# Kernel optimization log

Measured on AMD Instinct MI355X. Metric: run time of the kernel, lower is better.

The kernel has to match this reference:

```python
import jax, jax.numpy as jnp
import numpy as np

G, N_PER, D, H, L, IN_DIM = 128, 256, 256, 8, 3, 128
DH = D // H
EPS = 1e-5


def _ln(x, g, b):
    mu = jnp.mean(x, axis=-1, keepdims=True)
    var = jnp.mean(jnp.square(x - mu), axis=-1, keepdims=True)
    return (x - mu) * jax.lax.rsqrt(var + EPS) * g + b


def setup_inputs() -> dict:
    key = jax.random.key(0)
    ks = jax.random.split(key, 16)
    N = G * N_PER
    s = 0.02
    inp = {
        "x": jax.random.normal(ks[0], (N, IN_DIM), dtype=jnp.float32),
        "edge_index": jax.random.randint(ks[1], (2, 16 * N), 0, N, dtype=jnp.int32),
        "batch": (jnp.arange(N, dtype=jnp.int32) // N_PER),
        # input projection
        "Wp": jax.random.normal(ks[2], (D, IN_DIM), dtype=jnp.float32) * s,
        "bp": jnp.zeros((D,), jnp.float32),
        # per-layer stacked params (leading dim L)
        "in_w": jax.random.normal(ks[3], (L, 3 * D, D), dtype=jnp.float32) * s,
        "in_b": jnp.zeros((L, 3 * D), jnp.float32),
        "out_w": jax.random.normal(ks[4], (L, D, D), dtype=jnp.float32) * s,
        "out_b": jnp.zeros((L, D), jnp.float32),
        "n1_g": jnp.ones((L, D), jnp.float32),
        "n1_b": jnp.zeros((L, D), jnp.float32),
        "W1": jax.random.normal(ks[5], (L, 2 * D, D), dtype=jnp.float32) * s,
        "b1": jnp.zeros((L, 2 * D), jnp.float32),
        "W2": jax.random.normal(ks[6], (L, D, 2 * D), dtype=jnp.float32) * s,
        "b2": jnp.zeros((L, D), jnp.float32),
        "n2_g": jnp.ones((L, D), jnp.float32),
        "n2_b": jnp.zeros((L, D), jnp.float32),
        # final LayerNorm
        "ln_g": jnp.ones((D,), jnp.float32),
        "ln_b": jnp.zeros((D,), jnp.float32),
    }
    return inp


def _forward(x, Wp, bp, in_w, in_b, out_w, out_b, n1_g, n1_b, W1, b1, W2, b2, n2_g, n2_b, ln_g, ln_b):
    h = x @ Wp.T + bp                       # [N, D]
    h = h.reshape(G, N_PER, D)              # graphs are contiguous, equal size
    scale = 1.0 / np.sqrt(DH)
    for l in range(L):
        qkv = h @ in_w[l].T + in_b[l]       # [G, n, 3D]
        q, k, v = jnp.split(qkv, 3, axis=-1)
        q = q.reshape(G, N_PER, H, DH)
        k = k.reshape(G, N_PER, H, DH)
        v = v.reshape(G, N_PER, H, DH)
        scores = jnp.einsum('gqhd,gkhd->ghqk', q, k) * scale  # block-diag per graph
        attn = jax.nn.softmax(scores, axis=-1)
        o = jnp.einsum('ghqk,gkhd->gqhd', attn, v).reshape(G, N_PER, D)
        o = o @ out_w[l].T + out_b[l]
        h = _ln(h + o, n1_g[l], n1_b[l])
        f = jax.nn.relu(h @ W1[l].T + b1[l]) @ W2[l].T + b2[l]
        h = _ln(h + f, n2_g[l], n2_b[l])
    h = h.reshape(G * N_PER, D)
    return _ln(h, ln_g, ln_b)


def reference(x, edge_index, batch, Wp, bp, in_w, in_b, out_w, out_b, n1_g, n1_b, W1, b1, W2, b2, n2_g, n2_b, ln_g, ln_b):
    # edge_index and batch structure are honored: graphs are contiguous runs of
    # N_PER nodes, so the per-graph attention loop becomes batched block-diagonal attention.
    del edge_index, batch
    return _forward(x, Wp, bp, in_w, in_b, out_w, out_b, n1_g, n1_b, W1, b1, W2, b2, n2_g, n2_b, ln_g, ln_b)
```

## Files before the change

kernel.cpp:

```cpp
#include <hip/hip_runtime.h>

typedef unsigned short u16;
typedef unsigned long long u64;
typedef short bf16x8 __attribute__((ext_vector_type(8)));
typedef float f32x4 __attribute__((ext_vector_type(4)));

__device__ __forceinline__ u16 f2bf(float f) {
  union { float f; unsigned u; } v; v.f = f;
  unsigned r = v.u + 0x7fffu + ((v.u >> 16) & 1u);
  return (u16)(r >> 16);
}

__device__ __forceinline__ float bf2f(u16 b) {
  union { unsigned u; float f; } v; v.u = ((unsigned)b) << 16;
  return v.f;
}

__device__ __forceinline__ u64 pack4(float x, float y, float z, float w) {
  return (u64)f2bf(x) | ((u64)f2bf(y) << 16) |
         ((u64)f2bf(z) << 32) | ((u64)f2bf(w) << 48);
}

__device__ __forceinline__ float fexp2(float x) {
  float r; asm("v_exp_f32 %0, %1" : "=v"(r) : "v"(x)); return r;
}
__device__ __forceinline__ float frcp(float x) {
  float r; asm("v_rcp_f32 %0, %1" : "=v"(r) : "v"(x)); return r;
}

__device__ __forceinline__ void gld_lds16(const u16* g, u16* l) {
  __builtin_amdgcn_global_load_lds(
      (const __attribute__((address_space(1))) void*)g,
      (__attribute__((address_space(3))) void*)l, 16, 0, 0);
}

#define QSCALE (0.17677669529663687f * 1.44269504088896340f)

template<int MODE>
__global__ __launch_bounds__(256) void gemm_bt(
    const u16* __restrict__ A, const u16* __restrict__ B,
    const float* __restrict__ bias,
    u16* __restrict__ outb,
    int N, int K)
{
  __shared__ u16 As[128 * 64];
  __shared__ u16 Bs[128 * 64];
  const int tid = threadIdx.x;
  const int wave = tid >> 6, lane = tid & 63;
  const int quad = lane >> 4, l16 = lane & 15;

  const int nwg = gridDim.x * gridDim.y;
  int bid = blockIdx.y * gridDim.x + blockIdx.x;
  bid = (bid & 7) * (nwg >> 3) + (bid >> 3);
  const int by = bid / gridDim.x;
  const int bx = bid - by * gridDim.x;
  const int m0 = by * 128, n0 = bx * 128;

  const int wm = (wave >> 1) * 64, wn = (wave & 1) * 64;

  const int r0 = tid >> 3, ch0 = tid & 7;
  const int sc = ((ch0 ^ (r0 & 7)) * 8);

  const f32x4 zero = {0.f, 0.f, 0.f, 0.f};
  f32x4 acc[4][4];
#pragma unroll
  for (int i = 0; i < 4; i++)
#pragma unroll
    for (int j = 0; j < 4; j++) acc[i][j] = zero;

  const u16* Ap = A + (size_t)(m0 + r0) * K + sc;
  const u16* Bp = B + (size_t)(n0 + r0) * K + sc;
  u16* Asd = &As[tid * 8];
  u16* Bsd = &Bs[tid * 8];

  const int swz = (l16 & 7);

  for (int kt = 0; kt < K; kt += 64) {
#pragma unroll
    for (int p = 0; p < 4; p++) {
      gld_lds16(Ap + (size_t)(p * 32) * K + kt, Asd + p * 2048);
      gld_lds16(Bp + (size_t)(p * 32) * K + kt, Bsd + p * 2048);
    }
    __syncthreads();
#pragma unroll
    for (int kk = 0; kk < 2; kk++) {
      const int co = ((kk * 4 + quad) ^ swz) * 8;
      bf16x8 a[4], b[4];
#pragma unroll
      for (int i = 0; i < 4; i++)
        a[i] = *(const bf16x8*)&As[(wm + i * 16 + l16) * 64 + co];
#pragma unroll
      for (int j = 0; j < 4; j++)
        b[j] = *(const bf16x8*)&Bs[(wn + j * 16 + l16) * 64 + co];
#pragma unroll
      for (int i = 0; i < 4; i++)
#pragma unroll
        for (int j = 0; j < 4; j++)
          acc[i][j] = __builtin_amdgcn_mfma_f32_16x16x32_bf16(a[i], b[j], acc[i][j], 0, 0, 0);
    }
    __syncthreads();
  }

  float bj[4];
#pragma unroll
  for (int j = 0; j < 4; j++) bj[j] = bias[n0 + wn + j * 16 + l16];

#pragma unroll
  for (int i = 0; i < 4; i++) {
    const int Rb = m0 + wm + i * 16 + quad * 4;
#pragma unroll
    for (int r = 0; r < 4; r++) {
      const size_t ro = (size_t)(Rb + r) * N;
#pragma unroll
      for (int j = 0; j < 4; j++) {
        const int C = n0 + wn + j * 16 + l16;
        float v = acc[i][j][r] + bj[j];
        if (MODE == 1) {
          if (n0 + wn + j * 16 < 256) v *= QSCALE;
          outb[ro + C] = f2bf(v);
        } else if (MODE == 0) {
          outb[ro + C] = f2bf(v);
        } else {
          outb[ro + C] = f2bf(v > 0.f ? v : 0.f);
        }
      }
    }
  }
}

template<int FINAL>
__global__ __launch_bounds__(256) void gemm_ln(
    const u16* __restrict__ A, const u16* __restrict__ B,
    const float* __restrict__ bias, const u16* __restrict__ resb,
    const float* __restrict__ g1, const float* __restrict__ b1,
    const float* __restrict__ g2, const float* __restrict__ b2,
    float* __restrict__ outf, u16* __restrict__ outb,
    int K)
{
  __shared__ u16 As[64 * 64];
  __shared__ u16 Bs[256 * 64];
  __shared__ float Pp[FINAL ? 5 * 256 : 3 * 256];

  const int tid = threadIdx.x;
  const int wave = tid >> 6, lane = tid & 63;
  const int quad = lane >> 4, l16 = lane & 15;
  const int m0 = blockIdx.x * 64;

  if (tid < 256) {
    Pp[tid] = bias[tid];
    Pp[256 + tid] = g1[tid];
    Pp[512 + tid] = b1[tid];
    if (FINAL) {
      Pp[768 + tid] = g2[tid];
      Pp[1024 + tid] = b2[tid];
    }
  }

  const f32x4 zero = {0.f, 0.f, 0.f, 0.f};
  f32x4 acc[16];
#pragma unroll
  for (int j = 0; j < 16; j++) acc[j] = zero;

  const int r0 = tid >> 3, ch0 = tid & 7;
  const int sc = ((ch0 ^ (r0 & 7)) * 8);
  const u16* Ap = A + (size_t)(m0 + r0) * K + sc;
  const u16* Bp = B + (size_t)r0 * K + sc;
  u16* Asd = &As[tid * 8];
  u16* Bsd = &Bs[tid * 8];
  const int swz = (l16 & 7);

  for (int kt = 0; kt < K; kt += 64) {
#pragma unroll
    for (int p = 0; p < 2; p++)
      gld_lds16(Ap + (size_t)(p * 32) * K + kt, Asd + p * 2048);
#pragma unroll
    for (int p = 0; p < 8; p++)
      gld_lds16(Bp + (size_t)(p * 32) * K + kt, Bsd + p * 2048);
    __syncthreads();
#pragma unroll
    for (int kk = 0; kk < 2; kk++) {
      const int co = ((kk * 4 + quad) ^ swz) * 8;
      bf16x8 af = *(const bf16x8*)&As[(wave * 16 + l16) * 64 + co];
#pragma unroll
      for (int j = 0; j < 16; j++) {
        bf16x8 wf = *(const bf16x8*)&Bs[(j * 16 + l16) * 64 + co];
        acc[j] = __builtin_amdgcn_mfma_f32_16x16x32_bf16(wf, af, acc[j], 0, 0, 0);
      }
    }
    __syncthreads();
  }

  const int row = m0 + wave * 16 + l16;
  const int c4 = quad * 4;
  float s = 0.f, q = 0.f;
#pragma unroll
  for (int j = 0; j < 16; j++) {
    ushort4 rv = *(const ushort4*)(resb + (size_t)row * 256 + j * 16 + c4);
    float4 bv = *(const float4*)(Pp + j * 16 + c4);
    acc[j][0] += bv.x + bf2f(rv.x);
    acc[j][1] += bv.y + bf2f(rv.y);
    acc[j][2] += bv.z + bf2f(rv.z);
    acc[j][3] += bv.w + bf2f(rv.w);
    s += (acc[j][0] + acc[j][1]) + (acc[j][2] + acc[j][3]);
    q += (acc[j][0] * acc[j][0] + acc[j][1] * acc[j][1]) +
         (acc[j][2] * acc[j][2] + acc[j][3] * acc[j][3]);
  }
  s += __shfl_xor(s, 16, 64); s += __shfl_xor(s, 32, 64);
  q += __shfl_xor(q, 16, 64); q += __shfl_xor(q, 32, 64);
  float mu = s * 0.00390625f;
  float rs = rsqrtf(q * 0.00390625f - mu * mu + 1e-5f);

  if (FINAL == 0) {
#pragma unroll
    for (int j = 0; j < 16; j++) {
      float4 gv = *(const float4*)(Pp + 256 + j * 16 + c4);
      float4 bv = *(const float4*)(Pp + 512 + j * 16 + c4);
      float4 y;
      y.x = (acc[j][0] - mu) * rs * gv.x + bv.x;
      y.y = (acc[j][1] - mu) * rs * gv.y + bv.y;
      y.z = (acc[j][2] - mu) * rs * gv.z + bv.z;
      y.w = (acc[j][3] - mu) * rs * gv.w + bv.w;
      const size_t off = (size_t)row * 256 + j * 16 + c4;
      *(u64*)(outb + off) = pack4(y.x, y.y, y.z, y.w);
    }
  } else {
    float s2 = 0.f, q2 = 0.f;
#pragma unroll
    for (int j = 0; j < 16; j++) {
      float4 gv = *(const float4*)(Pp + 256 + j * 16 + c4);
      float4 bv = *(const float4*)(Pp + 512 + j * 16 + c4);
      acc[j][0] = (acc[j][0] - mu) * rs * gv.x + bv.x;
      acc[j][1] = (acc[j][1] - mu) * rs * gv.y + bv.y;
      acc[j][2] = (acc[j][2] - mu) * rs * gv.z + bv.z;
      acc[j][3] = (acc[j][3] - mu) * rs * gv.w + bv.w;
      s2 += (acc[j][0] + acc[j][1]) + (acc[j][2] + acc[j][3]);
      q2 += (acc[j][0] * acc[j][0] + acc[j][1] * acc[j][1]) +
            (acc[j][2] * acc[j][2] + acc[j][3] * acc[j][3]);
    }
    s2 += __shfl_xor(s2, 16, 64); s2 += __shfl_xor(s2, 32, 64);
    q2 += __shfl_xor(q2, 16, 64); q2 += __shfl_xor(q2, 32, 64);
    float mu2 = s2 * 0.00390625f;
    float rs2 = rsqrtf(q2 * 0.00390625f - mu2 * mu2 + 1e-5f);
#pragma unroll
    for (int j = 0; j < 16; j++) {
      float4 gv = *(const float4*)(Pp + 768 + j * 16 + c4);
      float4 bv = *(const float4*)(Pp + 1024 + j * 16 + c4);
      float4 z;
      z.x = (acc[j][0] - mu2) * rs2 * gv.x + bv.x;
      z.y = (acc[j][1] - mu2) * rs2 * gv.y + bv.y;
      z.z = (acc[j][2] - mu2) * rs2 * gv.z + bv.z;
      z.w = (acc[j][3] - mu2) * rs2 * gv.w + bv.w;
      *(float4*)(outf + (size_t)row * 256 + j * 16 + c4) = z;
    }
  }
}

__global__ __launch_bounds__(256) void attn_k(
    const u16* __restrict__ qkv, u16* __restrict__ ob)
{
  __shared__ u16 Ks[256 * 32];
  __shared__ u16 Vt[32 * 256];
  __shared__ u16 Pw[4][16 * 64];

  const int tid = threadIdx.x;
  const int wave = tid >> 6, lane = tid & 63;
  const int quad = lane >> 4, l16 = lane & 15;
  const int g = blockIdx.x >> 3, h = blockIdx.x & 7;
  const int node0 = g << 8;
  const int qoff = h * 32, koff = 256 + h * 32, voff = 512 + h * 32;

  {
    const int kr = tid >> 2, kc = (tid & 3) * 8;
    const u16* Kp = qkv + (size_t)(node0 + kr) * 768 + koff + kc;
    u16* Kd = &Ks[tid * 8];
#pragma unroll
    for (int pass = 0; pass < 4; pass++)
      gld_lds16(Kp + (size_t)pass * 64 * 768, Kd + pass * 2048);
  }

  {
    const int d = lane & 31;
    const int kb2 = lane >> 5;
#pragma unroll
    for (int t = 0; t < 4; t++) {
      const int kbg = wave * 8 + t * 2 + kb2;
      u16 vals[8];
#pragma unroll
      for (int i = 0; i < 8; i++)
        vals[i] = qkv[(size_t)(node0 + kbg * 8 + i) * 768 + voff + d];
      *(bf16x8*)&Vt[d * 256 + ((kbg ^ (d & 7)) << 3)] = *(bf16x8*)vals;
    }
  }

  __syncthreads();

  const f32x4 zero = {0.f, 0.f, 0.f, 0.f};
  bf16x8 ones;
#pragma unroll
  for (int i = 0; i < 8; i++) ones[i] = (short)0x3F80;
  u16* pw = Pw[wave];

  for (int qc = 0; qc < 4; qc++) {
    const int q0 = qc * 64 + wave * 16;

    bf16x8 qf = *(const bf16x8*)&qkv[(size_t)(node0 + q0 + l16) * 768 + qoff + quad * 8];

    f32x4 o[2] = {zero, zero};
    f32x4 ls = zero;

#pragma unroll
    for (int half = 0; half < 2; half++) {
      f32x4 s[8];
      __builtin_amdgcn_s_setprio(1);
#pragma unroll
      for (int ib = 0; ib < 8; ib++) {
        bf16x8 kf = *(const bf16x8*)&Ks[(half * 128 + ib * 16 + l16) * 32 + quad * 8];
        s[ib] = __builtin_amdgcn_mfma_f32_16x16x32_bf16(kf, qf, zero, 0, 0, 0);
      }
      __builtin_amdgcn_s_setprio(0);

#pragma unroll
      for (int Q = 0; Q < 2; Q++) {
#pragma unroll
        for (int ib = 0; ib < 4; ib++) {
          f32x4 p;
#pragma unroll
          for (int r = 0; r < 4; r++) p[r] = fexp2(s[Q * 4 + ib][r]);
          union { float f; unsigned u; } u0, u1, u2, u3;
          u0.f = p[0]; u1.f = p[1]; u2.f = p[2]; u3.f = p[3];
          uint2 pk;
          pk.x = __builtin_amdgcn_perm(u1.u, u0.u, 0x07060302u);
          pk.y = __builtin_amdgcn_perm(u3.u, u2.u, 0x07060302u);
          const int c = 2 * ib + (quad >> 1);
          *(uint2*)&pw[l16 * 64 + ((c ^ (l16 & 7)) << 3) + (quad & 1) * 4] = pk;
        }
#pragma unroll
        for (int ks = 0; ks < 2; ks++) {
          bf16x8 pf = *(const bf16x8*)&pw[l16 * 64 + (((ks * 4 + quad) ^ (l16 & 7)) << 3)];
          __builtin_amdgcn_s_setprio(1);
#pragma unroll
          for (int ib2 = 0; ib2 < 2; ib2++) {
            const int d = ib2 * 16 + l16;
            const int chunk = half * 16 + Q * 8 + ks * 4 + quad;
            bf16x8 vf = *(const bf16x8*)&Vt[d * 256 + ((chunk ^ (d & 7)) << 3)];
            o[ib2] = __builtin_amdgcn_mfma_f32_16x16x32_bf16(vf, pf, o[ib2], 0, 0, 0);
          }
          ls = __builtin_amdgcn_mfma_f32_16x16x32_bf16(ones, pf, ls, 0, 0, 0);
          __builtin_amdgcn_s_setprio(0);
        }
      }
    }

    const float inv = frcp(ls[0]);
    const size_t rowbase = (size_t)(node0 + q0 + l16) * 256 + h * 32;
#pragma unroll
    for (int ib2 = 0; ib2 < 2; ib2++) {
      u64 pk = pack4(o[ib2][0] * inv, o[ib2][1] * inv, o[ib2][2] * inv, o[ib2][3] * inv);
      *(u64*)&ob[rowbase + ib2 * 16 + quad * 4] = pk;
    }
  }
}

__global__ __launch_bounds__(256) void cvt_k(
    const float* __restrict__ s0, const float* __restrict__ s1,
    const float* __restrict__ s2, const float* __restrict__ s3,
    const float* __restrict__ s4, const float* __restrict__ s5,
    u16* __restrict__ d0, u16* __restrict__ d1, u16* __restrict__ d2,
    u16* __restrict__ d3, u16* __restrict__ d4, u16* __restrict__ d5)
{
  int t = (blockIdx.x * 256 + threadIdx.x) * 4;
  const float* s; u16* d; int off;
  if (t < 4194304)      { s = s0; d = d0; off = t; }
  else if (t < 4227072) { s = s1; d = d1; off = t - 4194304; }
  else if (t < 4816896) { s = s2; d = d2; off = t - 4227072; }
  else if (t < 5013504) { s = s3; d = d3; off = t - 4816896; }
  else if (t < 5406720) { s = s4; d = d4; off = t - 5013504; }
  else                  { s = s5; d = d5; off = t - 5406720; }
  float4 v = *(const float4*)(s + off);
  *(u64*)(d + off) = pack4(v.x, v.y, v.z, v.w);
}

extern "C" void kernel_launch(void* const* d_in, const int* in_sizes, int n_in,
                              void* d_out, int out_size, void* d_ws, size_t ws_size,
                              hipStream_t stream) {
  const float* x     = (const float*)d_in[0];
  const float* Wp    = (const float*)d_in[3];
  const float* bp    = (const float*)d_in[4];
  const float* in_w  = (const float*)d_in[5];
  const float* in_b  = (const float*)d_in[6];
  const float* out_w = (const float*)d_in[7];
  const float* out_b = (const float*)d_in[8];
  const float* n1_g  = (const float*)d_in[9];
  const float* n1_b  = (const float*)d_in[10];
  const float* W1    = (const float*)d_in[11];
  const float* b1    = (const float*)d_in[12];
  const float* W2    = (const float*)d_in[13];
  const float* b2    = (const float*)d_in[14];
  const float* n2_g  = (const float*)d_in[15];
  const float* n2_b  = (const float*)d_in[16];
  const float* ln_g  = (const float*)d_in[17];
  const float* ln_b  = (const float*)d_in[18];
  float* out = (float*)d_out;

  if (ws_size < 100000000u) return;

  char* ws = (char*)d_ws;
  u16* hb  = (u16*)(ws);
  u16* ob  = (u16*)(ws + 16777216);
  u16* mid = (u16*)(ws + 33554432);
  u16* wb  = (u16*)(ws + 83886080);
  u16* xb  = (u16*)(ws + 87097344);

  u16* Wpb   = wb;
  u16* inwb  = wb + 32768;
  u16* outwb = wb + 622592;
  u16* W1b   = wb + 819200;
  u16* W2b   = wb + 1212416;

  cvt_k<<<5664, 256, 0, stream>>>(x, Wp, in_w, out_w, W1, W2,
                                  xb, Wpb, inwb, outwb, W1b, W2b);

  gemm_bt<0><<<dim3(2, 256), 256, 0, stream>>>(xb, Wpb, bp, hb, 256, 128);

  for (int l = 0; l < 3; l++) {
    gemm_bt<1><<<dim3(6, 256), 256, 0, stream>>>(hb, inwb + l * 196608, in_b + l * 768,
                                                 mid, 768, 256);
    attn_k<<<1024, 256, 0, stream>>>(mid, ob);
    gemm_ln<0><<<512, 256, 0, stream>>>(ob, outwb + l * 65536, out_b + l * 256,
                                        hb, n1_g + l * 256, n1_b + l * 256,
                                        nullptr, nullptr, nullptr, hb, 256);
    gemm_bt<3><<<dim3(4, 256), 256, 0, stream>>>(hb, W1b + l * 131072, b1 + l * 512,
                                                 mid, 512, 256);
    if (l < 2) {
      gemm_ln<0><<<512, 256, 0, stream>>>(mid, W2b + l * 131072, b2 + l * 256,
                                          hb, n2_g + l * 256, n2_b + l * 256,
                                          nullptr, nullptr, nullptr, hb, 512);
    } else {
      gemm_ln<1><<<512, 256, 0, stream>>>(mid, W2b + l * 131072, b2 + l * 256,
                                          hb, n2_g + l * 256, n2_b + l * 256,
                                          ln_g, ln_b, out, nullptr, 512);
    }
  }
}
```

Measured before the change: 449.8 us.

## Triple-buffer gemm_ln K loop, prefetch residual, and prefetch next Q in attention

The GEMM+LayerNorm kernel now stages 32-wide K tiles into three LDS buffers with async global-to-LDS loads. Explicit vmcnt waits let loads for later tiles overlap MFMA work on the current one, replacing the previous load-sync-compute-sync loop. The residual row is loaded into registers before the GEMM so its latency is hidden. In attention, the next query chunk's Q fragment is prefetched while the current chunk computes. The cost is more register pressure from 16 residual ushort4s and more LDS, and the K tiles drop the XOR swizzle, which may cause bank conflicts.

```diff
diff --git a/kernel.cpp b/kernel.cpp
--- a/kernel.cpp
+++ b/kernel.cpp
@@ -128,17 +128,16 @@
   }
 }
 
-template<int FINAL>
+template<int FINAL, int KK>
 __global__ __launch_bounds__(256) void gemm_ln(
     const u16* __restrict__ A, const u16* __restrict__ B,
     const float* __restrict__ bias, const u16* __restrict__ resb,
     const float* __restrict__ g1, const float* __restrict__ b1,
     const float* __restrict__ g2, const float* __restrict__ b2,
-    float* __restrict__ outf, u16* __restrict__ outb,
-    int K)
+    float* __restrict__ outf, u16* __restrict__ outb)
 {
-  __shared__ u16 As[64 * 64];
-  __shared__ u16 Bs[256 * 64];
+  __shared__ u16 As[3][64 * 32];
+  __shared__ u16 Bs[3][256 * 32];
   __shared__ float Pp[FINAL ? 5 * 256 : 3 * 256];
 
   const int tid = threadIdx.x;
@@ -146,7 +145,7 @@
   const int quad = lane >> 4, l16 = lane & 15;
   const int m0 = blockIdx.x * 64;
 
-  if (tid < 256) {
+  {
     Pp[tid] = bias[tid];
     Pp[256 + tid] = g1[tid];
     Pp[512 + tid] = b1[tid];
@@ -156,51 +155,63 @@
     }
   }
 
+  const int row = m0 + wave * 16 + l16;
+  const int c4 = quad * 4;
+  ushort4 rv[16];
+#pragma unroll
+  for (int j = 0; j < 16; j++)
+    rv[j] = *(const ushort4*)(resb + (size_t)row * 256 + j * 16 + c4);
+
   const f32x4 zero = {0.f, 0.f, 0.f, 0.f};
   f32x4 acc[16];
 #pragma unroll
   for (int j = 0; j < 16; j++) acc[j] = zero;
 
-  const int r0 = tid >> 3, ch0 = tid & 7;
-  const int sc = ((ch0 ^ (r0 & 7)) * 8);
-  const u16* Ap = A + (size_t)(m0 + r0) * K + sc;
-  const u16* Bp = B + (size_t)r0 * K + sc;
-  u16* Asd = &As[tid * 8];
-  u16* Bsd = &Bs[tid * 8];
-  const int swz = (l16 & 7);
-
-  for (int kt = 0; kt < K; kt += 64) {
-#pragma unroll
-    for (int p = 0; p < 2; p++)
-      gld_lds16(Ap + (size_t)(p * 32) * K + kt, Asd + p * 2048);
-#pragma unroll
-    for (int p = 0; p < 8; p++)
-      gld_lds16(Bp + (size_t)(p * 32) * K + kt, Bsd + p * 2048);
-    __syncthreads();
-#pragma unroll
-    for (int kk = 0; kk < 2; kk++) {
-      const int co = ((kk * 4 + quad) ^ swz) * 8;
-      bf16x8 af = *(const bf16x8*)&As[(wave * 16 + l16) * 64 + co];
-#pragma unroll
-      for (int j = 0; j < 16; j++) {
-        bf16x8 wf = *(const bf16x8*)&Bs[(j * 16 + l16) * 64 + co];
-        acc[j] = __builtin_amdgcn_mfma_f32_16x16x32_bf16(wf, af, acc[j], 0, 0, 0);
-      }
-    }
-    __syncthreads();
-  }
-
-  const int row = m0 + wave * 16 + l16;
-  const int c4 = quad * 4;
+  const int r0 = tid >> 2, c0 = (tid & 3) * 8;
+  const u16* Ap = A + (size_t)(m0 + r0) * KK + c0;
+  const u16* Bp = B + (size_t)r0 * KK + c0;
+
+  auto stage = [&](int buf, int kt) {
+    gld_lds16(Ap + kt, &As[buf][tid * 8]);
+#pragma unroll
+    for (int p = 0; p < 4; p++)
+      gld_lds16(Bp + (size_t)(p * 64) * KK + kt, &Bs[buf][tid * 8 + p * 2048]);
+  };
+  auto compute = [&](int buf) {
+    bf16x8 af = *(const bf16x8*)&As[buf][(wave * 16 + l16) * 32 + quad * 8];
+#pragma unroll
+    for (int j = 0; j < 16; j++) {
+      bf16x8 wf = *(const bf16x8*)&Bs[buf][(j * 16 + l16) * 32 + quad * 8];
+      acc[j] = __builtin_amdgcn_mfma_f32_16x16x32_bf16(wf, af, acc[j], 0, 0, 0);
+    }
+  };
+
+  constexpr int NT = KK / 32;
+  stage(0, 0);
+  stage(1, 32);
+  stage(2, 64);
+#pragma unroll
+  for (int t = 0; t < NT; t++) {
+    if (t < NT - 2)      asm volatile("s_waitcnt vmcnt(10)" ::: "memory");
+    else if (t == NT - 2) asm volatile("s_waitcnt vmcnt(5)" ::: "memory");
+    else                  asm volatile("s_waitcnt vmcnt(0)" ::: "memory");
+    __builtin_amdgcn_sched_barrier(0);
+    __builtin_amdgcn_s_barrier();
+    compute(t % 3);
+    if (t < NT - 3) {
+      __builtin_amdgcn_s_barrier();
+      stage(t % 3, (t + 3) * 32);
+    }
+  }
+
   float s = 0.f, q = 0.f;
 #pragma unroll
   for (int j = 0; j < 16; j++) {
-    ushort4 rv = *(const ushort4*)(resb + (size_t)row * 256 + j * 16 + c4);
     float4 bv = *(const float4*)(Pp + j * 16 + c4);
-    acc[j][0] += bv.x + bf2f(rv.x);
-    acc[j][1] += bv.y + bf2f(rv.y);
-    acc[j][2] += bv.z + bf2f(rv.z);
-    acc[j][3] += bv.w + bf2f(rv.w);
+    acc[j][0] += bv.x + bf2f(rv[j].x);
+    acc[j][1] += bv.y + bf2f(rv[j].y);
+    acc[j][2] += bv.z + bf2f(rv[j].z);
+    acc[j][3] += bv.w + bf2f(rv[j].w);
     s += (acc[j][0] + acc[j][1]) + (acc[j][2] + acc[j][3]);
     q += (acc[j][0] * acc[j][0] + acc[j][1] * acc[j][1]) +
          (acc[j][2] * acc[j][2] + acc[j][3] * acc[j][3]);
@@ -300,10 +311,15 @@
   for (int i = 0; i < 8; i++) ones[i] = (short)0x3F80;
   u16* pw = Pw[wave];
 
+  bf16x8 qf = *(const bf16x8*)&qkv[(size_t)(node0 + wave * 16 + l16) * 768 + qoff + quad * 8];
+
+#pragma unroll
   for (int qc = 0; qc < 4; qc++) {
     const int q0 = qc * 64 + wave * 16;
 
-    bf16x8 qf = *(const bf16x8*)&qkv[(size_t)(node0 + q0 + l16) * 768 + qoff + quad * 8];
+    bf16x8 qnext = qf;
+    if (qc < 3)
+      qnext = *(const bf16x8*)&qkv[(size_t)(node0 + q0 + 64 + l16) * 768 + qoff + quad * 8];
 
     f32x4 o[2] = {zero, zero};
     f32x4 ls = zero;
@@ -358,6 +374,7 @@
       u64 pk = pack4(o[ib2][0] * inv, o[ib2][1] * inv, o[ib2][2] * inv, o[ib2][3] * inv);
       *(u64*)&ob[rowbase + ib2 * 16 + quad * 4] = pk;
     }
+    qf = qnext;
   }
 }
 
@@ -426,19 +443,19 @@
     gemm_bt<1><<<dim3(6, 256), 256, 0, stream>>>(hb, inwb + l * 196608, in_b + l * 768,
                                                  mid, 768, 256);
     attn_k<<<1024, 256, 0, stream>>>(mid, ob);
-    gemm_ln<0><<<512, 256, 0, stream>>>(ob, outwb + l * 65536, out_b + l * 256,
-                                        hb, n1_g + l * 256, n1_b + l * 256,
-                                        nullptr, nullptr, nullptr, hb, 256);
+    gemm_ln<0, 256><<<512, 256, 0, stream>>>(ob, outwb + l * 65536, out_b + l * 256,
+                                             hb, n1_g + l * 256, n1_b + l * 256,
+                                             nullptr, nullptr, nullptr, hb);
     gemm_bt<3><<<dim3(4, 256), 256, 0, stream>>>(hb, W1b + l * 131072, b1 + l * 512,
                                                  mid, 512, 256);
     if (l < 2) {
-      gemm_ln<0><<<512, 256, 0, stream>>>(mid, W2b + l * 131072, b2 + l * 256,
-                                          hb, n2_g + l * 256, n2_b + l * 256,
-                                          nullptr, nullptr, nullptr, hb, 512);
+      gemm_ln<0, 512><<<512, 256, 0, stream>>>(mid, W2b + l * 131072, b2 + l * 256,
+                                               hb, n2_g + l * 256, n2_b + l * 256,
+                                               nullptr, nullptr, nullptr, hb);
     } else {
-      gemm_ln<1><<<512, 256, 0, stream>>>(mid, W2b + l * 131072, b2 + l * 256,
-                                          hb, n2_g + l * 256, n2_b + l * 256,
-                                          ln_g, ln_b, out, nullptr, 512);
-    }
-  }
-}
+      gemm_ln<1, 512><<<512, 256, 0, stream>>>(mid, W2b + l * 131072, b2 + l * 256,
+                                               hb, n2_g + l * 256, n2_b + l * 256,
+                                               ln_g, ln_b, out, nullptr);
+    }
+  }
+}
```

After: 449.5 us. No clear change (-0.1%).

## Retile gemm_ln waves as 32x128 and prefetch residual and next Q fragment

Applied to the files above, without the earlier changes.

The fused GEMM+LayerNorm kernel changes its wave tiling from 16 rows by 256 columns to 32 rows by 128 columns. Each B fragment now feeds two MFMAs, which cuts LDS reads per MFMA, and row statistics are combined across the two column halves through shared memory plus an extra barrier. The residual tile is loaded before the K loop so its latency overlaps the GEMM, and K becomes a template constant. In attention, the next Q fragment is prefetched during the current query chunk; this adds register pressure and barrier overhead.

```diff
diff --git a/kernel.cpp b/kernel.cpp
--- a/kernel.cpp
+++ b/kernel.cpp
@@ -128,25 +128,30 @@
   }
 }
 
-template<int FINAL>
+template<int FINAL, int KK>
 __global__ __launch_bounds__(256) void gemm_ln(
     const u16* __restrict__ A, const u16* __restrict__ B,
     const float* __restrict__ bias, const u16* __restrict__ resb,
     const float* __restrict__ g1, const float* __restrict__ b1,
     const float* __restrict__ g2, const float* __restrict__ b2,
-    float* __restrict__ outf, u16* __restrict__ outb,
-    int K)
+    float* __restrict__ outf, u16* __restrict__ outb)
 {
   __shared__ u16 As[64 * 64];
   __shared__ u16 Bs[256 * 64];
   __shared__ float Pp[FINAL ? 5 * 256 : 3 * 256];
+  __shared__ float2 LN1[2][16][2][2];
+  __shared__ float2 LN2[2][16][2][2];
 
   const int tid = threadIdx.x;
   const int wave = tid >> 6, lane = tid & 63;
   const int quad = lane >> 4, l16 = lane & 15;
   const int m0 = blockIdx.x * 64;
-
-  if (tid < 256) {
+  const int rg = wave >> 1;
+  const int chf = wave & 1;
+  const int cb = chf * 128;
+  const int c4 = quad * 4;
+
+  {
     Pp[tid] = bias[tid];
     Pp[256 + tid] = g1[tid];
     Pp[512 + tid] = b1[tid];
@@ -156,101 +161,150 @@
     }
   }
 
+  const int row0 = m0 + rg * 32 + l16;
+  ushort4 rv[2][8];
+#pragma unroll
+  for (int i = 0; i < 2; i++)
+#pragma unroll
+    for (int j = 0; j < 8; j++)
+      rv[i][j] = *(const ushort4*)(resb + (size_t)(row0 + i * 16) * 256 + cb + j * 16 + c4);
+
   const f32x4 zero = {0.f, 0.f, 0.f, 0.f};
-  f32x4 acc[16];
-#pragma unroll
-  for (int j = 0; j < 16; j++) acc[j] = zero;
+  f32x4 acc[2][8];
+#pragma unroll
+  for (int i = 0; i < 2; i++)
+#pragma unroll
+    for (int j = 0; j < 8; j++) acc[i][j] = zero;
 
   const int r0 = tid >> 3, ch0 = tid & 7;
   const int sc = ((ch0 ^ (r0 & 7)) * 8);
-  const u16* Ap = A + (size_t)(m0 + r0) * K + sc;
-  const u16* Bp = B + (size_t)r0 * K + sc;
+  const u16* Ap = A + (size_t)(m0 + r0) * KK + sc;
+  const u16* Bp = B + (size_t)r0 * KK + sc;
   u16* Asd = &As[tid * 8];
   u16* Bsd = &Bs[tid * 8];
   const int swz = (l16 & 7);
 
-  for (int kt = 0; kt < K; kt += 64) {
+  for (int kt = 0; kt < KK; kt += 64) {
 #pragma unroll
     for (int p = 0; p < 2; p++)
-      gld_lds16(Ap + (size_t)(p * 32) * K + kt, Asd + p * 2048);
+      gld_lds16(Ap + (size_t)(p * 32) * KK + kt, Asd + p * 2048);
 #pragma unroll
     for (int p = 0; p < 8; p++)
-      gld_lds16(Bp + (size_t)(p * 32) * K + kt, Bsd + p * 2048);
+      gld_lds16(Bp + (size_t)(p * 32) * KK + kt, Bsd + p * 2048);
     __syncthreads();
 #pragma unroll
     for (int kk = 0; kk < 2; kk++) {
       const int co = ((kk * 4 + quad) ^ swz) * 8;
-      bf16x8 af = *(const bf16x8*)&As[(wave * 16 + l16) * 64 + co];
-#pragma unroll
-      for (int j = 0; j < 16; j++) {
-        bf16x8 wf = *(const bf16x8*)&Bs[(j * 16 + l16) * 64 + co];
-        acc[j] = __builtin_amdgcn_mfma_f32_16x16x32_bf16(wf, af, acc[j], 0, 0, 0);
+      bf16x8 af[2];
+#pragma unroll
+      for (int i = 0; i < 2; i++)
+        af[i] = *(const bf16x8*)&As[(rg * 32 + i * 16 + l16) * 64 + co];
+#pragma unroll
+      for (int j = 0; j < 8; j++) {
+        bf16x8 wf = *(const bf16x8*)&Bs[(cb + j * 16 + l16) * 64 + co];
+#pragma unroll
+        for (int i = 0; i < 2; i++)
+          acc[i][j] = __builtin_amdgcn_mfma_f32_16x16x32_bf16(wf, af[i], acc[i][j], 0, 0, 0);
       }
     }
     __syncthreads();
   }
 
-  const int row = m0 + wave * 16 + l16;
-  const int c4 = quad * 4;
-  float s = 0.f, q = 0.f;
-#pragma unroll
-  for (int j = 0; j < 16; j++) {
-    ushort4 rv = *(const ushort4*)(resb + (size_t)row * 256 + j * 16 + c4);
-    float4 bv = *(const float4*)(Pp + j * 16 + c4);
-    acc[j][0] += bv.x + bf2f(rv.x);
-    acc[j][1] += bv.y + bf2f(rv.y);
-    acc[j][2] += bv.z + bf2f(rv.z);
-    acc[j][3] += bv.w + bf2f(rv.w);
-    s += (acc[j][0] + acc[j][1]) + (acc[j][2] + acc[j][3]);
-    q += (acc[j][0] * acc[j][0] + acc[j][1] * acc[j][1]) +
-         (acc[j][2] * acc[j][2] + acc[j][3] * acc[j][3]);
-  }
-  s += __shfl_xor(s, 16, 64); s += __shfl_xor(s, 32, 64);
-  q += __shfl_xor(q, 16, 64); q += __shfl_xor(q, 32, 64);
-  float mu = s * 0.00390625f;
-  float rs = rsqrtf(q * 0.00390625f - mu * mu + 1e-5f);
+  float sa[2] = {0.f, 0.f}, qa[2] = {0.f, 0.f};
+#pragma unroll
+  for (int i = 0; i < 2; i++)
+#pragma unroll
+    for (int j = 0; j < 8; j++) {
+      float4 bv = *(const float4*)(Pp + cb + j * 16 + c4);
+      acc[i][j][0] += bv.x + bf2f(rv[i][j].x);
+      acc[i][j][1] += bv.y + bf2f(rv[i][j].y);
+      acc[i][j][2] += bv.z + bf2f(rv[i][j].z);
+      acc[i][j][3] += bv.w + bf2f(rv[i][j].w);
+      sa[i] += (acc[i][j][0] + acc[i][j][1]) + (acc[i][j][2] + acc[i][j][3]);
+      qa[i] += (acc[i][j][0] * acc[i][j][0] + acc[i][j][1] * acc[i][j][1]) +
+               (acc[i][j][2] * acc[i][j][2] + acc[i][j][3] * acc[i][j][3]);
+    }
+#pragma unroll
+  for (int i = 0; i < 2; i++) {
+    sa[i] += __shfl_xor(sa[i], 16, 64); sa[i] += __shfl_xor(sa[i], 32, 64);
+    qa[i] += __shfl_xor(qa[i], 16, 64); qa[i] += __shfl_xor(qa[i], 32, 64);
+  }
+  if (lane < 16) {
+#pragma unroll
+    for (int i = 0; i < 2; i++)
+      LN1[rg][lane][i][chf] = float2{sa[i], qa[i]};
+  }
+  __syncthreads();
+  float mu[2], rs[2];
+#pragma unroll
+  for (int i = 0; i < 2; i++) {
+    float2 o = LN1[rg][l16][i][chf ^ 1];
+    float ts = sa[i] + o.x, tq = qa[i] + o.y;
+    mu[i] = ts * 0.00390625f;
+    rs[i] = rsqrtf(tq * 0.00390625f - mu[i] * mu[i] + 1e-5f);
+  }
 
   if (FINAL == 0) {
 #pragma unroll
-    for (int j = 0; j < 16; j++) {
-      float4 gv = *(const float4*)(Pp + 256 + j * 16 + c4);
-      float4 bv = *(const float4*)(Pp + 512 + j * 16 + c4);
-      float4 y;
-      y.x = (acc[j][0] - mu) * rs * gv.x + bv.x;
-      y.y = (acc[j][1] - mu) * rs * gv.y + bv.y;
-      y.z = (acc[j][2] - mu) * rs * gv.z + bv.z;
-      y.w = (acc[j][3] - mu) * rs * gv.w + bv.w;
-      const size_t off = (size_t)row * 256 + j * 16 + c4;
-      *(u64*)(outb + off) = pack4(y.x, y.y, y.z, y.w);
+    for (int i = 0; i < 2; i++) {
+      const size_t rb = (size_t)(row0 + i * 16) * 256;
+#pragma unroll
+      for (int j = 0; j < 8; j++) {
+        float4 gv = *(const float4*)(Pp + 256 + cb + j * 16 + c4);
+        float4 bv = *(const float4*)(Pp + 512 + cb + j * 16 + c4);
+        float4 y;
+        y.x = (acc[i][j][0] - mu[i]) * rs[i] * gv.x + bv.x;
+        y.y = (acc[i][j][1] - mu[i]) * rs[i] * gv.y + bv.y;
+        y.z = (acc[i][j][2] - mu[i]) * rs[i] * gv.z + bv.z;
+        y.w = (acc[i][j][3] - mu[i]) * rs[i] * gv.w + bv.w;
+        *(u64*)(outb + rb + cb + j * 16 + c4) = pack4(y.x, y.y, y.z, y.w);
+      }
     }
   } else {
-    float s2 = 0.f, q2 = 0.f;
-#pragma unroll
-    for (int j = 0; j < 16; j++) {
-      float4 gv = *(const float4*)(Pp + 256 + j * 16 + c4);
-      float4 bv = *(const float4*)(Pp + 512 + j * 16 + c4);
-      acc[j][0] = (acc[j][0] - mu) * rs * gv.x + bv.x;
-      acc[j][1] = (acc[j][1] - mu) * rs * gv.y + bv.y;
-      acc[j][2] = (acc[j][2] - mu) * rs * gv.z + bv.z;
-      acc[j][3] = (acc[j][3] - mu) * rs * gv.w + bv.w;
-      s2 += (acc[j][0] + acc[j][1]) + (acc[j][2] + acc[j][3]);
-      q2 += (acc[j][0] * acc[j][0] + acc[j][1] * acc[j][1]) +
-            (acc[j][2] * acc[j][2] + acc[j][3] * acc[j][3]);
-    }
-    s2 += __shfl_xor(s2, 16, 64); s2 += __shfl_xor(s2, 32, 64);
-    q2 += __shfl_xor(q2, 16, 64); q2 += __shfl_xor(q2, 32, 64);
-    float mu2 = s2 * 0.00390625f;
-    float rs2 = rsqrtf(q2 * 0.00390625f - mu2 * mu2 + 1e-5f);
-#pragma unroll
-    for (int j = 0; j < 16; j++) {
-      float4 gv = *(const float4*)(Pp + 768 + j * 16 + c4);
-      float4 bv = *(const float4*)(Pp + 1024 + j * 16 + c4);
-      float4 z;
-      z.x = (acc[j][0] - mu2) * rs2 * gv.x + bv.x;
-      z.y = (acc[j][1] - mu2) * rs2 * gv.y + bv.y;
-      z.z = (acc[j][2] - mu2) * rs2 * gv.z + bv.z;
-      z.w = (acc[j][3] - mu2) * rs2 * gv.w + bv.w;
-      *(float4*)(outf + (size_t)row * 256 + j * 16 + c4) = z;
+    float s2[2] = {0.f, 0.f}, q2[2] = {0.f, 0.f};
+#pragma unroll
+    for (int i = 0; i < 2; i++)
+#pragma unroll
+      for (int j = 0; j < 8; j++) {
+        float4 gv = *(const float4*)(Pp + 256 + cb + j * 16 + c4);
+        float4 bv = *(const float4*)(Pp + 512 + cb + j * 16 + c4);
+        acc[i][j][0] = (acc[i][j][0] - mu[i]) * rs[i] * gv.x + bv.x;
+        acc[i][j][1] = (acc[i][j][1] - mu[i]) * rs[i] * gv.y + bv.y;
+        acc[i][j][2] = (acc[i][j][2] - mu[i]) * rs[i] * gv.z + bv.z;
+        acc[i][j][3] = (acc[i][j][3] - mu[i]) * rs[i] * gv.w + bv.w;
+        s2[i] += (acc[i][j][0] + acc[i][j][1]) + (acc[i][j][2] + acc[i][j][3]);
+        q2[i] += (acc[i][j][0] * acc[i][j][0] + acc[i][j][1] * acc[i][j][1]) +
+                 (acc[i][j][2] * acc[i][j][2] + acc[i][j][3] * acc[i][j][3]);
+      }
+#pragma unroll
+    for (int i = 0; i < 2; i++) {
+      s2[i] += __shfl_xor(s2[i], 16, 64); s2[i] += __shfl_xor(s2[i], 32, 64);
+      q2[i] += __shfl_xor(q2[i], 16, 64); q2[i] += __shfl_xor(q2[i], 32, 64);
+    }
+    if (lane < 16) {
+#pragma unroll
+      for (int i = 0; i < 2; i++)
+        LN2[rg][lane][i][chf] = float2{s2[i], q2[i]};
+    }
+    __syncthreads();
+#pragma unroll
+    for (int i = 0; i < 2; i++) {
+      float2 o = LN2[rg][l16][i][chf ^ 1];
+      float ts = s2[i] + o.x, tq = q2[i] + o.y;
+      float mu2 = ts * 0.00390625f;
+      float rs2 = rsqrtf(tq * 0.00390625f - mu2 * mu2 + 1e-5f);
+      const size_t rb = (size_t)(row0 + i * 16) * 256;
+#pragma unroll
+      for (int j = 0; j < 8; j++) {
+        float4 gv = *(const float4*)(Pp + 768 + cb + j * 16 + c4);
+        float4 bv = *(const float4*)(Pp + 1024 + cb + j * 16 + c4);
+        float4 z;
+        z.x = (acc[i][j][0] - mu2) * rs2 * gv.x + bv.x;
+        z.y = (acc[i][j][1] - mu2) * rs2 * gv.y + bv.y;
+        z.z = (acc[i][j][2] - mu2) * rs2 * gv.z + bv.z;
+        z.w = (acc[i][j][3] - mu2) * rs2 * gv.w + bv.w;
+        *(float4*)(outf + rb + cb + j * 16 + c4) = z;
+      }
     }
   }
 }
@@ -300,10 +354,15 @@
   for (int i = 0; i < 8; i++) ones[i] = (short)0x3F80;
   u16* pw = Pw[wave];
 
+  bf16x8 qf = *(const bf16x8*)&qkv[(size_t)(node0 + wave * 16 + l16) * 768 + qoff + quad * 8];
+
+#pragma unroll
   for (int qc = 0; qc < 4; qc++) {
     const int q0 = qc * 64 + wave * 16;
 
-    bf16x8 qf = *(const bf16x8*)&qkv[(size_t)(node0 + q0 + l16) * 768 + qoff + quad * 8];
+    bf16x8 qnext = qf;
+    if (qc < 3)
+      qnext = *(const bf16x8*)&qkv[(size_t)(node0 + q0 + 64 + l16) * 768 + qoff + quad * 8];
 
     f32x4 o[2] = {zero, zero};
     f32x4 ls = zero;
@@ -358,6 +417,7 @@
       u64 pk = pack4(o[ib2][0] * inv, o[ib2][1] * inv, o[ib2][2] * inv, o[ib2][3] * inv);
       *(u64*)&ob[rowbase + ib2 * 16 + quad * 4] = pk;
     }
+    qf = qnext;
   }
 }
 
@@ -426,19 +486,19 @@
     gemm_bt<1><<<dim3(6, 256), 256, 0, stream>>>(hb, inwb + l * 196608, in_b + l * 768,
                                                  mid, 768, 256);
     attn_k<<<1024, 256, 0, stream>>>(mid, ob);
-    gemm_ln<0><<<512, 256, 0, stream>>>(ob, outwb + l * 65536, out_b + l * 256,
-                                        hb, n1_g + l * 256, n1_b + l * 256,
-                                        nullptr, nullptr, nullptr, hb, 256);
+    gemm_ln<0, 256><<<512, 256, 0, stream>>>(ob, outwb + l * 65536, out_b + l * 256,
+                                             hb, n1_g + l * 256, n1_b + l * 256,
+                                             nullptr, nullptr, nullptr, hb);
     gemm_bt<3><<<dim3(4, 256), 256, 0, stream>>>(hb, W1b + l * 131072, b1 + l * 512,
                                                  mid, 512, 256);
     if (l < 2) {
-      gemm_ln<0><<<512, 256, 0, stream>>>(mid, W2b + l * 131072, b2 + l * 256,
-                                          hb, n2_g + l * 256, n2_b + l * 256,
-                                          nullptr, nullptr, nullptr, hb, 512);
+      gemm_ln<0, 512><<<512, 256, 0, stream>>>(mid, W2b + l * 131072, b2 + l * 256,
+                                               hb, n2_g + l * 256, n2_b + l * 256,
+                                               nullptr, nullptr, nullptr, hb);
     } else {
-      gemm_ln<1><<<512, 256, 0, stream>>>(mid, W2b + l * 131072, b2 + l * 256,
-                                          hb, n2_g + l * 256, n2_b + l * 256,
-                                          ln_g, ln_b, out, nullptr, 512);
-    }
-  }
-}
+      gemm_ln<1, 512><<<512, 256, 0, stream>>>(mid, W2b + l * 131072, b2 + l * 256,
+                                               hb, n2_g + l * 256, n2_b + l * 256,
+                                               ln_g, ln_b, out, nullptr);
+    }
+  }
+}
```

After: 483.7 us. 7.5% more time.
